# Performance work log

Measured on AMD Instinct MI355X. Metric: run time of the kernel, lower is better.

## Reference

```python
import jax, jax.numpy as jnp
import numpy as np

BATCH = 8192
IN_FEATURES = 128
OUT_FEATURES = 256
GRID_SIZE = 20
ORDER = 3
L = GRID_SIZE + ORDER  # coeffs length per edge = 23


def setup_inputs() -> dict:
    key = jax.random.key(0)
    kx, kc = jax.random.split(key)
    x = jax.random.normal(kx, (BATCH, IN_FEATURES), dtype=jnp.float32)
    # fused per-edge B-spline coefficients: [out_features, in_features, grid_size+order]
    coeffs = jax.random.normal(kc, (OUT_FEATURES, IN_FEATURES, L), dtype=jnp.float32) * 0.1
    return {"x": x, "coeffs": coeffs}


def reference(x, coeffs):
    # x: [B, I], coeffs: [O, I, L]
    O, I, Lc = coeffs.shape
    B = x.shape[0]
    s = jax.nn.sigmoid(x)                      # x_clamped in (0, 1)
    idx = s * (GRID_SIZE - 1)                  # fractional bin index in [0, 19)
    k = idx.astype(jnp.int32)                  # trunc == floor since idx >= 0
    w1 = idx - k.astype(x.dtype)
    w0 = 1.0 - w1
    k0 = jnp.clip(k, 0, Lc - 1)                # [B, I]
    k1 = jnp.clip(k + 1, 0, Lc - 1)
    # Build sparse interpolation weights [B, I, L] (two nonzeros per (b, j)),
    # then contract against the shared coefficient tensor in one fused reduce:
    # out[b, i] = sum_j c[i, j, k0[b,j]] * w0[b,j] + c[i, j, k1[b,j]] * w1[b,j]
    brow = jnp.arange(B)[:, None]
    jcol = jnp.arange(I)[None, :]
    W = jnp.zeros((B, I, Lc), dtype=x.dtype)
    W = W.at[brow, jcol, k0].add(w0)
    W = W.at[brow, jcol, k1].add(w1)
    return jnp.einsum('bjl,ijl->bi', W, coeffs)  # [B, O]
```

## Files before the change

### kernel.cpp

```cpp
#include <hip/hip_runtime.h>
#include <hip/hip_fp16.h>

#define BATCH 8192
#define IN_F 128
#define OUT_F 256
#define LC 23
#define BROW 768
#define JPW 16

typedef _Float16 f16x8 __attribute__((ext_vector_type(8)));
typedef float f32x4 __attribute__((ext_vector_type(4)));
typedef _Float16 half2v __attribute__((ext_vector_type(2)));

__global__ __launch_bounds__(256) void prep_kernel(
    const float* __restrict__ coeffs, _Float16* __restrict__ cp2) {
    int t = blockIdx.x * 256 + threadIdx.x;
    int col = t & 15;
    int u = t >> 4;
    int q = u % 3;
    int v = u / 3;
    int g = v & 15;
    int j = v >> 4;
    int i = g * 16 + col;
    int s0 = q * 8;
    const float* src = coeffs + ((size_t)i * IN_F + j) * LC;
    f16x8 w;
#pragma unroll
    for (int e = 0; e < 8; ++e) {
        int s = s0 + e;
        float f = (s < 20) ? src[s] : 0.0f;
        w[e] = (_Float16)f;
    }
    char* dst = reinterpret_cast<char*>(cp2) +
                (size_t)(j * 16 + g) * BROW + q * 256 + col * 16;
    *reinterpret_cast<f16x8*>(dst) = w;
}

__global__ __launch_bounds__(512, 4) void kan_mfma8(
    const float* __restrict__ x, const char* __restrict__ cp2,
    float* __restrict__ out) {
    __shared__ uint2 mlds[IN_F][64];

    const int tid = threadIdx.x;
    const int lane = tid & 63;
    const int ks = tid >> 6;
    const int l15 = lane & 15;
    const int q = lane >> 4;
    const int q4 = q * 4;
    const int qc = (q < 3) ? q : 2;

    int wg = (blockIdx.x & 7) * 64 + (blockIdx.x >> 3);
    const int mb = wg >> 2;
    const int bn = wg & 3;
    const int b0 = mb * 64;

    {
        const int row = lane;
        const int jb = ks * 16;
        const float4* xr = reinterpret_cast<const float4*>(
            x + (size_t)(b0 + row) * IN_F + jb);
#pragma unroll
        for (int u = 0; u < 4; ++u) {
            float4 xv = xr[u];
#pragma unroll
            for (int e = 0; e < 4; ++e) {
                float xvv = (e == 0) ? xv.x : (e == 1) ? xv.y
                           : (e == 2) ? xv.z : xv.w;
                float s = 1.0f / (1.0f + __expf(-xvv));
                float idxf = s * 19.0f;
                int k = (int)idxf;
                k = (k > 18) ? 18 : k;
                float w1 = idxf - (float)k;
                float w0 = 1.0f - w1;
                unsigned u0 = __half_as_ushort(__float2half(w0));
                unsigned u1 = __half_as_ushort(__float2half(w1));
                unsigned lo, hi;
                if (k & 1) { lo = u0 << 16; hi = u1; }
                else       { lo = u0 | (u1 << 16); hi = 0u; }
                unsigned P = (unsigned)(k >> 1);
                mlds[jb + u * 4 + e][row] = uint2{lo, hi | (P << 16)};
            }
        }
    }
    __syncthreads();

    const int j0 = ks * JPW;
    const char* bbase = cp2 + (size_t)(bn * 4) * BROW + qc * 256 + l15 * 16;
    auto bld = [&](int j, int nf) {
        return *reinterpret_cast<const f16x8*>(
            bbase + (size_t)(j * 16 + nf) * BROW);
    };

    f32x4 acc[4][4];
#pragma unroll
    for (int mf = 0; mf < 4; ++mf)
#pragma unroll
        for (int nf = 0; nf < 4; ++nf) acc[mf][nf] = f32x4{0.f, 0.f, 0.f, 0.f};

    f16x8 rc[4], rn[4];
#pragma unroll
    for (int h = 0; h < 4; ++h) rc[h] = bld(j0, h);

    auto step = [&](f16x8 (&cur)[4], f16x8 (&nxt)[4], int j, int jn) {
#pragma unroll
        for (int h = 0; h < 4; ++h) nxt[h] = bld(jn, h);
#pragma unroll
        for (int mf = 0; mf < 4; ++mf) {
            uint2 m = mlds[j][mf * 16 + l15];
            unsigned lo = m.x;
            unsigned hi = m.y & 0xFFFFu;
            int d = (int)(m.y >> 16) - q4;
            union { uint32_t u[4]; f16x8 h; } au;
#pragma unroll
            for (int r = 0; r < 4; ++r) {
                uint32_t v = (d == r) ? lo : 0u;
                v = (d == r - 1) ? hi : v;
                au.u[r] = v;
            }
#pragma unroll
            for (int nf = 0; nf < 4; ++nf)
                acc[mf][nf] = __builtin_amdgcn_mfma_f32_16x16x32_f16(
                    au.h, cur[nf], acc[mf][nf], 0, 0, 0);
        }
    };

    for (int jj = 0; jj < JPW; jj += 2) {
        step(rc, rn, j0 + jj, j0 + jj + 1);
        step(rn, rc, j0 + jj + 1, j0 + ((jj + 2) & (JPW - 1)));
    }

    __syncthreads();
    float* red = reinterpret_cast<float*>(&mlds[0][0]);
#pragma unroll
    for (int p = 0; p < 2; ++p) {
        if (p) __syncthreads();
#pragma unroll
        for (int mf = 0; mf < 4; ++mf)
#pragma unroll
            for (int t = 0; t < 2; ++t)
#pragma unroll
                for (int r = 0; r < 4; ++r) {
                    int colsw = (t * 16 + l15 + (q & 1) * 16) & 31;
                    red[ks * 2048 + (mf * 16 + q4 + r) * 32 + colsw] =
                        acc[mf][p * 2 + t][r];
                }
        __syncthreads();
#pragma unroll
        for (int it = 0; it < 4; ++it) {
            int idx = it * 512 + tid;
            int row = idx >> 5;
            int col = idx & 31;
            int colsw = (col + ((row >> 2) & 1) * 16) & 31;
            float s = 0.f;
#pragma unroll
            for (int w = 0; w < 8; ++w) s += red[w * 2048 + row * 32 + colsw];
            out[(size_t)(b0 + row) * OUT_F + bn * 64 + p * 32 + col] = s;
        }
    }
}

__device__ __forceinline__ float dot2_acc(unsigned cbits, unsigned wbits,
                                          float acc) {
#if __has_builtin(__builtin_amdgcn_fdot2)
    union { unsigned u; half2v h; } c, w;
    c.u = cbits; w.u = wbits;
    return __builtin_amdgcn_fdot2(c.h, w.h, acc, false);
#else
    __half2 hc = *reinterpret_cast<const __half2*>(&cbits);
    __half2 hw = *reinterpret_cast<const __half2*>(&wbits);
    float2 fc = __half22float2(hc);
    float2 fw = __half22float2(hw);
    return acc + fc.x * fw.x + fc.y * fw.y;
#endif
}

__global__ __launch_bounds__(256) void build_ctg_kernel(
    const float* __restrict__ coeffs, unsigned short* __restrict__ ctg) {
    int tid = blockIdx.x * 256 + threadIdx.x;
    int qq = tid & 63;
    int k = (tid >> 6) % LC;
    int j = tid / (64 * LC);
    if (j >= IN_F) return;
    int k1 = (k + 1 < LC) ? (k + 1) : (LC - 1);
    union { unsigned short h[8]; uint4 v; } u;
#pragma unroll
    for (int c = 0; c < 4; ++c) {
        int i = qq * 4 + c;
        const float* base = coeffs + ((size_t)i * IN_F + j) * LC;
        u.h[2 * c]     = __half_as_ushort(__float2half(base[k]));
        u.h[2 * c + 1] = __half_as_ushort(__float2half(base[k1]));
    }
    reinterpret_cast<uint4*>(ctg)[tid] = u.v;
}

__global__ __launch_bounds__(256) void kan_main_kernel(
    const float* __restrict__ x, const char* __restrict__ ctg,
    float* __restrict__ out) {
    __shared__ unsigned metas[4][2 * IN_F];
    const int wave = threadIdx.x >> 6;
    const int lane = threadIdx.x & 63;
    const int b = blockIdx.x * 4 + wave;
    float2 xv = reinterpret_cast<const float2*>(x + (size_t)b * IN_F)[lane];
    uint4 m;
#pragma unroll
    for (int t = 0; t < 2; ++t) {
        float xs = t ? xv.y : xv.x;
        float s = 1.0f / (1.0f + __expf(-xs));
        float idxf = s * 19.0f;
        int k = (int)idxf;
        k = (k > 18) ? 18 : k;
        float w1 = idxf - (float)k;
        float w0 = 1.0f - w1;
        int j = 2 * lane + t;
        unsigned off = (unsigned)((j * LC + k) << 10);
        half2v w; w[0] = (_Float16)w0; w[1] = (_Float16)w1;
        unsigned wbits = *reinterpret_cast<unsigned*>(&w);
        if (t == 0) { m.x = off; m.y = wbits; }
        else        { m.z = off; m.w = wbits; }
    }
    reinterpret_cast<uint4*>(&metas[wave][0])[lane] = m;
    __syncthreads();
    const unsigned lanebase = lane * 16;
    const uint4* mrow = reinterpret_cast<const uint4*>(&metas[wave][0]);
    float acc0 = 0.f, acc1 = 0.f, acc2 = 0.f, acc3 = 0.f;
#pragma unroll 8
    for (int j2 = 0; j2 < IN_F / 2; ++j2) {
        uint4 mm = mrow[j2];
        {
            const uint4 e = *reinterpret_cast<const uint4*>(
                ctg + (size_t)(lanebase + mm.x));
            acc0 = dot2_acc(e.x, mm.y, acc0);
            acc1 = dot2_acc(e.y, mm.y, acc1);
            acc2 = dot2_acc(e.z, mm.y, acc2);
            acc3 = dot2_acc(e.w, mm.y, acc3);
        }
        {
            const uint4 e = *reinterpret_cast<const uint4*>(
                ctg + (size_t)(lanebase + mm.z));
            acc0 = dot2_acc(e.x, mm.w, acc0);
            acc1 = dot2_acc(e.y, mm.w, acc1);
            acc2 = dot2_acc(e.z, mm.w, acc2);
            acc3 = dot2_acc(e.w, mm.w, acc3);
        }
    }
    float4 r = make_float4(acc0, acc1, acc2, acc3);
    reinterpret_cast<float4*>(out + (size_t)b * OUT_F)[lane] = r;
}

extern "C" void kernel_launch(void* const* d_in, const int* in_sizes, int n_in,
                              void* d_out, int out_size, void* d_ws,
                              size_t ws_size, hipStream_t stream) {
    const float* x = (const float*)d_in[0];
    const float* coeffs = (const float*)d_in[1];
    float* out = (float*)d_out;

    const size_t cp2_bytes = (size_t)IN_F * 16 * BROW;
    const size_t ctg_bytes = (size_t)IN_F * LC * 64 * 16;

    if (d_ws != nullptr && ws_size >= cp2_bytes) {
        _Float16* cp2 = (_Float16*)d_ws;
        prep_kernel<<<384, 256, 0, stream>>>(coeffs, cp2);
        kan_mfma8<<<512, 512, 0, stream>>>(x, (const char*)cp2, out);
    } else if (d_ws != nullptr && ws_size >= ctg_bytes) {
        char* ctg = (char*)d_ws;
        const int totalA = IN_F * LC * 64;
        build_ctg_kernel<<<(totalA + 255) / 256, 256, 0, stream>>>(
            coeffs, (unsigned short*)ctg);
        kan_main_kernel<<<BATCH / 4, 256, 0, stream>>>(x, ctg, out);
    } else {
        kan_main_kernel<<<BATCH / 4, 256, 0, stream>>>(x, (const char*)d_ws,
                                                       out);
    }
}
```

Before: 30.18 us.

## Pack K dimension densely across features to cut wasted MFMA work

Coefficients are repacked so the reduction axis is a flat sequence of 20 spline slots per input feature, grouped into 80 blocks of 32, instead of padding each feature to 24 slots. Each wave now walks 10 dense K-blocks rather than 16 padded per-feature blocks, which cuts MFMA count and B-operand loads. Because a K-block can span up to three features, the A fragment is assembled from three LDS entries with extra compare/select logic per lane.

```diff
diff --git a/kernel.cpp b/kernel.cpp
--- a/kernel.cpp
+++ b/kernel.cpp
@@ -5,39 +5,35 @@
 #define IN_F 128
 #define OUT_F 256
 #define LC 23
-#define BROW 768
-#define JPW 16
+#define NKB 80
+#define KBPW 10
 
 typedef _Float16 f16x8 __attribute__((ext_vector_type(8)));
 typedef float f32x4 __attribute__((ext_vector_type(4)));
 typedef _Float16 half2v __attribute__((ext_vector_type(2)));
 
-__global__ __launch_bounds__(256) void prep_kernel(
-    const float* __restrict__ coeffs, _Float16* __restrict__ cp2) {
+__global__ __launch_bounds__(256) void prep_kernel9(
+    const float* __restrict__ coeffs, char* __restrict__ cp3) {
     int t = blockIdx.x * 256 + threadIdx.x;
     int col = t & 15;
-    int u = t >> 4;
-    int q = u % 3;
-    int v = u / 3;
-    int g = v & 15;
-    int j = v >> 4;
+    int q = (t >> 4) & 3;
+    int g = (t >> 6) & 15;
+    int kb = t >> 10;
     int i = g * 16 + col;
-    int s0 = q * 8;
-    const float* src = coeffs + ((size_t)i * IN_F + j) * LC;
+    int fbase = kb * 32 + q * 8;
     f16x8 w;
 #pragma unroll
     for (int e = 0; e < 8; ++e) {
-        int s = s0 + e;
-        float f = (s < 20) ? src[s] : 0.0f;
-        w[e] = (_Float16)f;
-    }
-    char* dst = reinterpret_cast<char*>(cp2) +
-                (size_t)(j * 16 + g) * BROW + q * 256 + col * 16;
-    *reinterpret_cast<f16x8*>(dst) = w;
-}
-
-__global__ __launch_bounds__(512, 4) void kan_mfma8(
-    const float* __restrict__ x, const char* __restrict__ cp2,
+        int f = fbase + e;
+        int j = f / 20;
+        int s = f - 20 * j;
+        w[e] = (_Float16)coeffs[((size_t)i * IN_F + j) * LC + s];
+    }
+    *reinterpret_cast<f16x8*>(cp3 + (size_t)t * 16) = w;
+}
+
+__global__ __launch_bounds__(512, 4) void kan_mfma9(
+    const float* __restrict__ x, const char* __restrict__ cp3,
     float* __restrict__ out) {
     __shared__ uint2 mlds[IN_F][64];
 
@@ -47,7 +43,6 @@
     const int l15 = lane & 15;
     const int q = lane >> 4;
     const int q4 = q * 4;
-    const int qc = (q < 3) ? q : 2;
 
     int wg = (blockIdx.x & 7) * 64 + (blockIdx.x >> 3);
     const int mb = wg >> 2;
@@ -77,18 +72,19 @@
                 unsigned lo, hi;
                 if (k & 1) { lo = u0 << 16; hi = u1; }
                 else       { lo = u0 | (u1 << 16); hi = 0u; }
-                unsigned P = (unsigned)(k >> 1);
-                mlds[jb + u * 4 + e][row] = uint2{lo, hi | (P << 16)};
+                int j = jb + u * 4 + e;
+                unsigned p = (unsigned)(j * 10 + (k >> 1));
+                mlds[j][row] = uint2{lo, hi | (p << 16)};
             }
         }
     }
     __syncthreads();
 
-    const int j0 = ks * JPW;
-    const char* bbase = cp2 + (size_t)(bn * 4) * BROW + qc * 256 + l15 * 16;
-    auto bld = [&](int j, int nf) {
+    const int kb0 = ks * KBPW;
+    const char* bbase = cp3 + lane * 16;
+    auto bld = [&](int kb, int nf) {
         return *reinterpret_cast<const f16x8*>(
-            bbase + (size_t)(j * 16 + nf) * BROW);
+            bbase + ((size_t)((kb * 16 + bn * 4 + nf)) << 10));
     };
 
     f32x4 acc[4][4];
@@ -99,22 +95,37 @@
 
     f16x8 rc[4], rn[4];
 #pragma unroll
-    for (int h = 0; h < 4; ++h) rc[h] = bld(j0, h);
-
-    auto step = [&](f16x8 (&cur)[4], f16x8 (&nxt)[4], int j, int jn) {
-#pragma unroll
-        for (int h = 0; h < 4; ++h) nxt[h] = bld(jn, h);
+    for (int h = 0; h < 4; ++h) rc[h] = bld(kb0, h);
+
+    auto step = [&](f16x8 (&cur)[4], f16x8 (&nxt)[4], int kb, int kbn) {
+#pragma unroll
+        for (int h = 0; h < 4; ++h) nxt[h] = bld(kbn, h);
+        const int pwin = kb * 16;
+        const int base = pwin + q4;
+        const int j0 = pwin / 10;
+        const int jB = (j0 + 1 < IN_F - 1) ? j0 + 1 : IN_F - 1;
+        const int jC = (j0 + 2 < IN_F - 1) ? j0 + 2 : IN_F - 1;
 #pragma unroll
         for (int mf = 0; mf < 4; ++mf) {
-            uint2 m = mlds[j][mf * 16 + l15];
-            unsigned lo = m.x;
-            unsigned hi = m.y & 0xFFFFu;
-            int d = (int)(m.y >> 16) - q4;
+            const int row = mf * 16 + l15;
+            uint2 m0 = mlds[j0][row];
+            uint2 m1 = mlds[jB][row];
+            uint2 m2 = mlds[jC][row];
+            int d0 = (int)(m0.y >> 16) - base;
+            int d1 = (int)(m1.y >> 16) - base;
+            int d2 = (int)(m2.y >> 16) - base;
+            unsigned h0 = m0.y & 0xFFFFu, h1 = m1.y & 0xFFFFu,
+                     h2 = m2.y & 0xFFFFu;
             union { uint32_t u[4]; f16x8 h; } au;
 #pragma unroll
             for (int r = 0; r < 4; ++r) {
-                uint32_t v = (d == r) ? lo : 0u;
-                v = (d == r - 1) ? hi : v;
+                uint32_t v = 0u;
+                v = (d0 == r) ? m0.x : v;
+                v = (d0 == r - 1) ? h0 : v;
+                v = (d1 == r) ? m1.x : v;
+                v = (d1 == r - 1) ? h1 : v;
+                v = (d2 == r) ? m2.x : v;
+                v = (d2 == r - 1) ? h2 : v;
                 au.u[r] = v;
             }
 #pragma unroll
@@ -124,9 +135,10 @@
         }
     };
 
-    for (int jj = 0; jj < JPW; jj += 2) {
-        step(rc, rn, j0 + jj, j0 + jj + 1);
-        step(rn, rc, j0 + jj + 1, j0 + ((jj + 2) & (JPW - 1)));
+    for (int kk = 0; kk < KBPW; kk += 2) {
+        step(rc, rn, kb0 + kk, kb0 + kk + 1);
+        int kwrap = (kk + 2 < KBPW) ? (kb0 + kk + 2) : kb0;
+        step(rn, rc, kb0 + kk + 1, kwrap);
     }
 
     __syncthreads();
@@ -254,13 +266,13 @@
     const float* coeffs = (const float*)d_in[1];
     float* out = (float*)d_out;
 
-    const size_t cp2_bytes = (size_t)IN_F * 16 * BROW;
+    const size_t cp3_bytes = (size_t)NKB * 16 * 64 * 16;
     const size_t ctg_bytes = (size_t)IN_F * LC * 64 * 16;
 
-    if (d_ws != nullptr && ws_size >= cp2_bytes) {
-        _Float16* cp2 = (_Float16*)d_ws;
-        prep_kernel<<<384, 256, 0, stream>>>(coeffs, cp2);
-        kan_mfma8<<<512, 512, 0, stream>>>(x, (const char*)cp2, out);
+    if (d_ws != nullptr && ws_size >= cp3_bytes) {
+        char* cp3 = (char*)d_ws;
+        prep_kernel9<<<320, 256, 0, stream>>>(coeffs, cp3);
+        kan_mfma9<<<512, 512, 0, stream>>>(x, cp3, out);
     } else if (d_ws != nullptr && ws_size >= ctg_bytes) {
         char* ctg = (char*)d_ws;
         const int totalA = IN_F * LC * 64;
```

After: 36.02 us. 1.19x slower.

## Split waves into 2 row halves x 4 K-slices with deeper B prefetch

Applied to the files above, without the earlier changes.

The eight waves per block are regrouped from eight K-slices covering all 64 rows into two 32-row halves times four K-slices of 32 features each. Each wave holds half the accumulators (2x4 MFMA tiles instead of 4x4), and B fragments are loaded two steps ahead through four rotating register buffers. The cross-wave reduction drops from eight partials to four and runs in one pass over 64 columns. The cost is that each B fragment is now loaded by two waves instead of one, doubling global/L2 traffic for coefficients in exchange for fewer registers and a cheaper reduction.

```diff
diff --git a/kernel.cpp b/kernel.cpp
--- a/kernel.cpp
+++ b/kernel.cpp
@@ -6,7 +6,7 @@
 #define OUT_F 256
 #define LC 23
 #define BROW 768
-#define JPW 16
+#define JPW 32
 
 typedef _Float16 f16x8 __attribute__((ext_vector_type(8)));
 typedef float f32x4 __attribute__((ext_vector_type(4)));
@@ -36,14 +36,16 @@
     *reinterpret_cast<f16x8*>(dst) = w;
 }
 
-__global__ __launch_bounds__(512, 4) void kan_mfma8(
+__global__ __launch_bounds__(512, 4) void kan_mfma10(
     const float* __restrict__ x, const char* __restrict__ cp2,
     float* __restrict__ out) {
     __shared__ uint2 mlds[IN_F][64];
 
     const int tid = threadIdx.x;
     const int lane = tid & 63;
-    const int ks = tid >> 6;
+    const int wave = tid >> 6;
+    const int ks = wave & 3;
+    const int mh = wave >> 2;
     const int l15 = lane & 15;
     const int q = lane >> 4;
     const int q4 = q * 4;
@@ -56,7 +58,7 @@
 
     {
         const int row = lane;
-        const int jb = ks * 16;
+        const int jb = wave * 16;
         const float4* xr = reinterpret_cast<const float4*>(
             x + (size_t)(b0 + row) * IN_F + jb);
 #pragma unroll
@@ -86,27 +88,27 @@
 
     const int j0 = ks * JPW;
     const char* bbase = cp2 + (size_t)(bn * 4) * BROW + qc * 256 + l15 * 16;
-    auto bld = [&](int j, int nf) {
-        return *reinterpret_cast<const f16x8*>(
-            bbase + (size_t)(j * 16 + nf) * BROW);
+
+    f32x4 acc[2][4];
+#pragma unroll
+    for (int mf = 0; mf < 2; ++mf)
+#pragma unroll
+        for (int nf = 0; nf < 4; ++nf) acc[mf][nf] = f32x4{0.f, 0.f, 0.f, 0.f};
+
+    f16x8 B0[4], B1[4], B2[4], B3[4];
+
+    auto LOADJ = [&](f16x8 (&buf)[4], int jrel) {
+        const char* src = bbase + (size_t)((j0 + (jrel & (JPW - 1))) * 16) * BROW;
+#pragma unroll
+        for (int nf = 0; nf < 4; ++nf)
+            buf[nf] = *reinterpret_cast<const f16x8*>(src + nf * BROW);
     };
-
-    f32x4 acc[4][4];
-#pragma unroll
-    for (int mf = 0; mf < 4; ++mf)
-#pragma unroll
-        for (int nf = 0; nf < 4; ++nf) acc[mf][nf] = f32x4{0.f, 0.f, 0.f, 0.f};
-
-    f16x8 rc[4], rn[4];
-#pragma unroll
-    for (int h = 0; h < 4; ++h) rc[h] = bld(j0, h);
-
-    auto step = [&](f16x8 (&cur)[4], f16x8 (&nxt)[4], int j, int jn) {
-#pragma unroll
-        for (int h = 0; h < 4; ++h) nxt[h] = bld(jn, h);
-#pragma unroll
-        for (int mf = 0; mf < 4; ++mf) {
-            uint2 m = mlds[j][mf * 16 + l15];
+    auto STEP = [&](f16x8 (&cur)[4], f16x8 (&tgt)[4], int jc, int jl) {
+        LOADJ(tgt, jl);
+        const int j = j0 + jc;
+#pragma unroll
+        for (int mf = 0; mf < 2; ++mf) {
+            uint2 m = mlds[j][mh * 32 + mf * 16 + l15];
             unsigned lo = m.x;
             unsigned hi = m.y & 0xFFFFu;
             int d = (int)(m.y >> 16) - q4;
@@ -124,38 +126,41 @@
         }
     };
 
-    for (int jj = 0; jj < JPW; jj += 2) {
-        step(rc, rn, j0 + jj, j0 + jj + 1);
-        step(rn, rc, j0 + jj + 1, j0 + ((jj + 2) & (JPW - 1)));
+    LOADJ(B0, 0);
+    LOADJ(B1, 1);
+    for (int jj = 0; jj < JPW; jj += 4) {
+        STEP(B0, B2, jj + 0, jj + 2);
+        STEP(B1, B3, jj + 1, jj + 3);
+        STEP(B2, B0, jj + 2, jj + 4);
+        STEP(B3, B1, jj + 3, jj + 5);
     }
 
     __syncthreads();
     float* red = reinterpret_cast<float*>(&mlds[0][0]);
 #pragma unroll
-    for (int p = 0; p < 2; ++p) {
-        if (p) __syncthreads();
-#pragma unroll
-        for (int mf = 0; mf < 4; ++mf)
-#pragma unroll
-            for (int t = 0; t < 2; ++t)
-#pragma unroll
-                for (int r = 0; r < 4; ++r) {
-                    int colsw = (t * 16 + l15 + (q & 1) * 16) & 31;
-                    red[ks * 2048 + (mf * 16 + q4 + r) * 32 + colsw] =
-                        acc[mf][p * 2 + t][r];
-                }
-        __syncthreads();
-#pragma unroll
-        for (int it = 0; it < 4; ++it) {
-            int idx = it * 512 + tid;
-            int row = idx >> 5;
-            int col = idx & 31;
-            int colsw = (col + ((row >> 2) & 1) * 16) & 31;
-            float s = 0.f;
-#pragma unroll
-            for (int w = 0; w < 8; ++w) s += red[w * 2048 + row * 32 + colsw];
-            out[(size_t)(b0 + row) * OUT_F + bn * 64 + p * 32 + col] = s;
-        }
+    for (int mf = 0; mf < 2; ++mf)
+#pragma unroll
+        for (int nf = 0; nf < 4; ++nf)
+#pragma unroll
+            for (int r = 0; r < 4; ++r) {
+                int row32 = mf * 16 + q4 + r;
+                int colsw = (nf * 16 + l15 + q * 16) & 63;
+                red[(wave * 32 + row32) * 64 + colsw] = acc[mf][nf][r];
+            }
+    __syncthreads();
+#pragma unroll
+    for (int it = 0; it < 8; ++it) {
+        int idx = it * 512 + tid;
+        int row64 = idx >> 6;
+        int col = idx & 63;
+        int mhh = row64 >> 5;
+        int row32 = row64 & 31;
+        int colsw = (col + ((row32 >> 2) & 3) * 16) & 63;
+        float s = 0.f;
+#pragma unroll
+        for (int k = 0; k < 4; ++k)
+            s += red[((mhh * 4 + k) * 32 + row32) * 64 + colsw];
+        out[(size_t)(b0 + row64) * OUT_F + bn * 64 + col] = s;
     }
 }
 
@@ -260,7 +265,7 @@
     if (d_ws != nullptr && ws_size >= cp2_bytes) {
         _Float16* cp2 = (_Float16*)d_ws;
         prep_kernel<<<384, 256, 0, stream>>>(coeffs, cp2);
-        kan_mfma8<<<512, 512, 0, stream>>>(x, (const char*)cp2, out);
+        kan_mfma10<<<512, 512, 0, stream>>>(x, (const char*)cp2, out);
     } else if (d_ws != nullptr && ws_size >= ctg_bytes) {
         char* ctg = (char*)d_ws;
         const int totalA = IN_F * LC * 64;
```

Measured after the change: 32.47 us. 7.6% more time.
